# Performance work log

Measured on AMD Instinct MI355X. Metric: run time of the kernel, lower is better.

The kernel has to match this reference:

```python
import jax, jax.numpy as jnp
import numpy as np

B = 256      # batch size (molecules)
A = 64       # num_atoms per molecule
N = B * A    # total nodes = 16384
E = 262144   # num edges
H = 128      # hidden_dim
L = 4        # num_layers
LAT = 64     # latent_dim
AF = 16      # atom_feature_dim
LN_EPS = 1e-5


def setup_inputs() -> dict:
    key = jax.random.key(0)
    ks = jax.random.split(key, 26)
    w = lambda k, shape: (jax.random.normal(k, shape) * 0.05).astype(jnp.float32)
    inp = {}
    inp["z"] = jax.random.normal(ks[0], (B, LAT), jnp.float32)
    inp["atom_types"] = jax.nn.one_hot(
        jax.random.randint(ks[1], (N,), 0, AF), AF, dtype=jnp.float32)
    inp["pos0"] = jax.random.normal(ks[2], (N, 3), jnp.float32) * 0.1
    inp["edge_index"] = jax.random.randint(ks[3], (2, E), 0, N)
    # latent injector: Linear(LAT+AF, 2H) -> SiLU -> Linear(2H, H) -> SiLU -> Linear(H, H)
    inp["inj_W1"] = w(ks[4], (AF + LAT, 2 * H)); inp["inj_b1"] = jnp.zeros((2 * H,), jnp.float32)
    inp["inj_W2"] = w(ks[5], (2 * H, H));        inp["inj_b2"] = jnp.zeros((H,), jnp.float32)
    inp["inj_W3"] = w(ks[6], (H, H));            inp["inj_b3"] = jnp.zeros((H,), jnp.float32)
    # per-layer params, stacked over layer dim L
    inp["edge_W1"] = w(ks[7], (L, 2 * H + 1, H)); inp["edge_b1"] = jnp.zeros((L, H), jnp.float32)
    inp["edge_W2"] = w(ks[8], (L, H, H));         inp["edge_b2"] = jnp.zeros((L, H), jnp.float32)
    inp["coord_W1"] = w(ks[9], (L, H, H));        inp["coord_b1"] = jnp.zeros((L, H), jnp.float32)
    inp["coord_W2"] = w(ks[10], (L, H, 1))  # no bias
    inp["node_W1"] = w(ks[11], (L, 2 * H, H));    inp["node_b1"] = jnp.zeros((L, H), jnp.float32)
    inp["node_W2"] = w(ks[12], (L, H, H));        inp["node_b2"] = jnp.zeros((L, H), jnp.float32)
    inp["ln_g"] = jnp.ones((L, H), jnp.float32)
    inp["ln_b"] = jnp.zeros((L, H), jnp.float32)
    return inp


def _layer_norm(x, g, b):
    mu = jnp.mean(x, axis=-1, keepdims=True)
    var = jnp.mean((x - mu) ** 2, axis=-1, keepdims=True)
    return (x - mu) * jax.lax.rsqrt(var + LN_EPS) * g + b


def _egnn_layer(h, pos, row, col, eW1, eb1, eW2, eb2, cW1, cb1, cW2, nW1, nb1, nW2, nb2, g, b):
    # --- message: gather endpoints, edge MLP ---
    rel = pos[row] - pos[col]                                   # [E, 3]
    dsq = jnp.clip(jnp.sum(rel * rel, axis=1, keepdims=True), 1e-6, 1e6)  # [E, 1]
    ef = jnp.concatenate([h[row], h[col], dsq], axis=1)         # [E, 2H+1]
    m = jax.nn.silu(ef @ eW1 + eb1)
    m = jax.nn.silu(m @ eW2 + eb2)
    m = jnp.clip(m, -10.0, 10.0)                                # [E, H]
    # --- coordinate update: coord MLP -> weighted rel_pos -> scatter_add, mean-normalized ---
    cw = jax.nn.silu(m @ cW1 + cb1) @ cW2                       # [E, 1]
    coord_update = jax.ops.segment_sum(cw * rel, row, num_segments=N)   # [N, 3]
    num_neighbors = jax.ops.segment_sum(jnp.ones((row.shape[0],), m.dtype), row, num_segments=N)[:, None]
    pos_new = pos + coord_update / (num_neighbors + 1e-6)
    # --- node update: scatter_add messages, node MLP, residual + LayerNorm ---
    agg = jax.ops.segment_sum(m, row, num_segments=N)           # [N, H]
    nu = jnp.concatenate([h, agg], axis=1)                      # [N, 2H]
    nu = jax.nn.silu(nu @ nW1 + nb1) @ nW2 + nb2
    h_new = _layer_norm(h + nu, g, b)
    return h_new, pos_new


def reference(z, atom_types, pos0, edge_index,
              inj_W1, inj_b1, inj_W2, inj_b2, inj_W3, inj_b3,
              edge_W1, edge_b1, edge_W2, edge_b2,
              coord_W1, coord_b1, coord_W2,
              node_W1, node_b1, node_W2, node_b2,
              ln_g, ln_b):
    # latent injection: h = MLP(cat[atom_types, repeat_interleave(z, num_atoms)])
    z_exp = jnp.repeat(z, A, axis=0)                            # [N, LAT]
    h = jnp.concatenate([atom_types, z_exp], axis=1)            # [N, AF+LAT]
    h = jax.nn.silu(h @ inj_W1 + inj_b1)
    h = jax.nn.silu(h @ inj_W2 + inj_b2)
    h = h @ inj_W3 + inj_b3                                     # [N, H]
    pos = pos0
    row, col = edge_index[0], edge_index[1]
    for l in range(L):
        h, pos = _egnn_layer(h, pos, row, col,
                             edge_W1[l], edge_b1[l], edge_W2[l], edge_b2[l],
                             coord_W1[l], coord_b1[l], coord_W2[l],
                             node_W1[l], node_b1[l], node_W2[l], node_b2[l],
                             ln_g[l], ln_b[l])
    return pos
```

## Files before the change

### kernel.cpp

```cpp
#include <hip/hip_runtime.h>
#include <cmath>

#define N_NODES 16384
#define E_EDGES 262144
#define HD 128
#define NLAYER 4

typedef __attribute__((ext_vector_type(8))) short bf16x8;
typedef __attribute__((ext_vector_type(4))) float f32x4;
#define MFMA16(a, b, c) __builtin_amdgcn_mfma_f32_16x16x32_bf16(a, b, c, 0, 0, 0)

__device__ __forceinline__ float silu_f(float x) {
  return __fdividef(x, 1.0f + __expf(-x));
}

__device__ __forceinline__ unsigned short bf16_rn(float f) {
  union { float f; unsigned u; } v; v.f = f;
  unsigned r = (v.u + 0x7FFFu + ((v.u >> 16) & 1u)) >> 16;
  return (unsigned short)r;
}
__device__ __forceinline__ float bf16_tof(unsigned short h) {
  union { unsigned u; float f; } v; v.u = ((unsigned)h) << 16; return v.f;
}

__global__ void k_prep_w(const float* __restrict__ eW1, const float* __restrict__ eW2,
                         const float* __restrict__ cW1,
                         unsigned short* __restrict__ e1f, unsigned short* __restrict__ e2f,
                         unsigned short* __restrict__ c1f) {
  int sid = blockIdx.x * 256 + threadIdx.x;
  int layer = sid >> 13;
  int r = sid & 8191;
  const float* src; unsigned short* base; int c, s, halfstride;
  if (r < 4096) {
    c = r >> 9; s = r & 511;
    src = eW1 + (size_t)layer * 257 * 128;
    base = e1f + (size_t)layer * 65536; halfstride = 32768;
  } else if (r < 6144) {
    int rr = r - 4096; c = rr >> 9; s = rr & 511;
    src = eW2 + (size_t)layer * 128 * 128;
    base = e2f + (size_t)layer * 32768; halfstride = 16384;
  } else {
    int rr = r - 6144; c = rr >> 9; s = rr & 511;
    src = cW1 + (size_t)layer * 128 * 128;
    base = c1f + (size_t)layer * 32768; halfstride = 16384;
  }
  int cf = s >> 6, lp = s & 63;
  int n = cf * 16 + (lp & 15);
  int k0 = c * 32 + (lp >> 4) * 8;
  bf16x8 hv, lv;
#pragma unroll
  for (int j = 0; j < 8; ++j) {
    float w = src[(size_t)(k0 + j) * 128 + n];
    unsigned short h = bf16_rn(w);
    hv[j] = (short)h;
    lv[j] = (short)bf16_rn(w - bf16_tof(h));
  }
  size_t off = ((size_t)c * 512 + s) * 8;
  *(bf16x8*)(base + off) = hv;
  *(bf16x8*)(base + halfstride + off) = lv;
}

__global__ void k_h2bf(const float* __restrict__ h, unsigned short* __restrict__ hhi,
                       unsigned short* __restrict__ hlo) {
  int i = (blockIdx.x * 256 + threadIdx.x) * 8;
  float4 a = *(const float4*)(h + i), b = *(const float4*)(h + i + 4);
  float v[8] = {a.x, a.y, a.z, a.w, b.x, b.y, b.z, b.w};
  bf16x8 hv, lv;
#pragma unroll
  for (int j = 0; j < 8; ++j) {
    unsigned u = __float_as_uint(v[j]);
    hv[j] = (short)(u >> 16);
    float hi_f = __uint_as_float(u & 0xFFFF0000u);
    lv[j] = (short)bf16_rn(v[j] - hi_f);
  }
  *(bf16x8*)(hhi + i) = hv;
  *(bf16x8*)(hlo + i) = lv;
}

__global__ __launch_bounds__(256, 4) void k_edge_mfma(
    const unsigned short* __restrict__ hhi, const unsigned short* __restrict__ hlo,
    const float* __restrict__ pos,
    const int* __restrict__ rows, const int* __restrict__ cols, const int* __restrict__ perm,
    const unsigned short* __restrict__ e1f, const float* __restrict__ eW1,
    const float* __restrict__ eb1,
    const unsigned short* __restrict__ e2f, const float* __restrict__ eb2,
    const unsigned short* __restrict__ c1f, const float* __restrict__ cb1,
    const float* __restrict__ cW2,
    float* __restrict__ agg, float* __restrict__ coordacc) {
  __shared__ __align__(16) float T[64][132];
  __shared__ int srow[64], scol[64];
  __shared__ float sdsq[64];
  __shared__ float srel[64][4];

  const int tid = threadIdx.x;
  const int lane = tid & 63;
  const int w = tid >> 6;
  const int l15 = lane & 15, l4 = lane >> 4;
  const int j0 = blockIdx.x * 64;
  const f32x4 zero4 = {0.f, 0.f, 0.f, 0.f};

  if (tid < 64) {
    int e = perm[j0 + tid];
    int r = rows[e], c = cols[e];
    srow[tid] = r; scol[tid] = c;
    float rx = pos[r * 3 + 0] - pos[c * 3 + 0];
    float ry = pos[r * 3 + 1] - pos[c * 3 + 1];
    float rz = pos[r * 3 + 2] - pos[c * 3 + 2];
    srel[tid][0] = rx; srel[tid][1] = ry; srel[tid][2] = rz;
    float d = rx * rx + ry * ry + rz * rz;
    sdsq[tid] = fminf(fmaxf(d, 1e-6f), 1e6f);
  }
  __syncthreads();

  f32x4 acc[8];

#pragma unroll
  for (int i = 0; i < 8; ++i) acc[i] = zero4;
  for (int c = 0; c < 8; ++c) {
    int node = (c < 4 ? srow : scol)[16 * w + l15];
    int koff = (c & 3) * 32 + l4 * 8;
    bf16x8 ah = *(const bf16x8*)(hhi + (size_t)node * 128 + koff);
    bf16x8 al = *(const bf16x8*)(hlo + (size_t)node * 128 + koff);
    const unsigned short* b0 = e1f + (size_t)c * 4096 + (size_t)lane * 8;
#pragma unroll
    for (int cf = 0; cf < 8; ++cf) {
      bf16x8 bh = *(const bf16x8*)(b0 + cf * 512);
      bf16x8 bl = *(const bf16x8*)(b0 + 32768 + cf * 512);
      acc[cf] = MFMA16(ah, bh, acc[cf]);
      acc[cf] = MFMA16(al, bh, acc[cf]);
      acc[cf] = MFMA16(ah, bl, acc[cf]);
    }
  }
#pragma unroll
  for (int cf = 0; cf < 8; ++cf) {
    int col = cf * 16 + l15;
    float wl = eW1[256 * 128 + col];
    float bb = eb1[col];
#pragma unroll
    for (int r = 0; r < 4; ++r) {
      int trow = 16 * w + l4 * 4 + r;
      T[trow][col] = silu_f(acc[cf][r] + sdsq[trow] * wl + bb);
    }
  }

#pragma unroll
  for (int i = 0; i < 8; ++i) acc[i] = zero4;
  for (int c = 0; c < 4; ++c) {
    int trow = 16 * w + l15;
    int k0 = c * 32 + l4 * 8;
    float tv[8];
    *(float4*)(tv) = *(const float4*)(&T[trow][k0]);
    *(float4*)(tv + 4) = *(const float4*)(&T[trow][k0 + 4]);
    bf16x8 ah, al;
#pragma unroll
    for (int j = 0; j < 8; ++j) {
      unsigned u = __float_as_uint(tv[j]);
      ah[j] = (short)(u >> 16);
      float hi_f = __uint_as_float(u & 0xFFFF0000u);
      al[j] = (short)bf16_rn(tv[j] - hi_f);
    }
    const unsigned short* b0 = e2f + (size_t)c * 4096 + (size_t)lane * 8;
#pragma unroll
    for (int cf = 0; cf < 8; ++cf) {
      bf16x8 bh = *(const bf16x8*)(b0 + cf * 512);
      bf16x8 bl = *(const bf16x8*)(b0 + 16384 + cf * 512);
      acc[cf] = MFMA16(ah, bh, acc[cf]);
      acc[cf] = MFMA16(al, bh, acc[cf]);
      acc[cf] = MFMA16(ah, bl, acc[cf]);
    }
  }
#pragma unroll
  for (int cf = 0; cf < 8; ++cf) {
    int col = cf * 16 + l15;
    float bb = eb2[col];
#pragma unroll
    for (int r = 0; r < 4; ++r) {
      int trow = 16 * w + l4 * 4 + r;
      float v = silu_f(acc[cf][r] + bb);
      v = fminf(fmaxf(v, -10.0f), 10.0f);
      acc[cf][r] = v;
      T[trow][col] = v;
    }
  }
  {
    int seg = 0;
    while (seg < 16) {
      int node = srow[16 * w + seg];
      int se = seg + 1;
      while (se < 16 && srow[16 * w + se] == node) ++se;
#pragma unroll
      for (int cf = 0; cf < 8; ++cf) {
        float s = 0.f;
#pragma unroll
        for (int r = 0; r < 4; ++r) {
          int row = l4 * 4 + r;
          s += (row >= seg && row < se) ? acc[cf][r] : 0.f;
        }
        s += __shfl_xor(s, 16);
        s += __shfl_xor(s, 32);
        if (l4 == 0) atomicAdd(&agg[(size_t)node * 128 + cf * 16 + l15], s);
      }
      seg = se;
    }
  }

#pragma unroll
  for (int i = 0; i < 8; ++i) acc[i] = zero4;
  for (int c = 0; c < 4; ++c) {
    int trow = 16 * w + l15;
    int k0 = c * 32 + l4 * 8;
    float tv[8];
    *(float4*)(tv) = *(const float4*)(&T[trow][k0]);
    *(float4*)(tv + 4) = *(const float4*)(&T[trow][k0 + 4]);
    bf16x8 ah, al;
#pragma unroll
    for (int j = 0; j < 8; ++j) {
      unsigned u = __float_as_uint(tv[j]);
      ah[j] = (short)(u >> 16);
      float hi_f = __uint_as_float(u & 0xFFFF0000u);
      al[j] = (short)bf16_rn(tv[j] - hi_f);
    }
    const unsigned short* b0 = c1f + (size_t)c * 4096 + (size_t)lane * 8;
#pragma unroll
    for (int cf = 0; cf < 8; ++cf) {
      bf16x8 bh = *(const bf16x8*)(b0 + cf * 512);
      bf16x8 bl = *(const bf16x8*)(b0 + 16384 + cf * 512);
      acc[cf] = MFMA16(ah, bh, acc[cf]);
      acc[cf] = MFMA16(al, bh, acc[cf]);
      acc[cf] = MFMA16(ah, bl, acc[cf]);
    }
  }
  {
    float p[4] = {0.f, 0.f, 0.f, 0.f};
#pragma unroll
    for (int cf = 0; cf < 8; ++cf) {
      int col = cf * 16 + l15;
      float bb = cb1[col];
      float w2 = cW2[col];
#pragma unroll
      for (int r = 0; r < 4; ++r) p[r] += silu_f(acc[cf][r] + bb) * w2;
    }
#pragma unroll
    for (int d = 1; d < 16; d <<= 1) {
#pragma unroll
      for (int r = 0; r < 4; ++r) p[r] += __shfl_xor(p[r], d);
    }
    int seg = 0;
    while (seg < 16) {
      int node = srow[16 * w + seg];
      int se = seg + 1;
      while (se < 16 && srow[16 * w + se] == node) ++se;
      float s = 0.f;
      if (l15 < 3) {
#pragma unroll
        for (int r = 0; r < 4; ++r) {
          int row = l4 * 4 + r;
          s += (row >= seg && row < se) ? p[r] * srel[16 * w + row][l15] : 0.f;
        }
      }
      s += __shfl_xor(s, 16);
      s += __shfl_xor(s, 32);
      if (l4 == 0 && l15 < 3) atomicAdd(&coordacc[(size_t)node * 4 + l15], s);
      seg = se;
    }
  }
}

__global__ void k_pos_fin(const float* __restrict__ coordacc, const int* __restrict__ offs,
                          float* __restrict__ pos) {
  int n = blockIdx.x * 256 + threadIdx.x;
  if (n < N_NODES) {
    float deg = (float)(offs[n + 1] - offs[n]);
    float inv = __fdividef(1.0f, deg + 1e-6f);
    pos[n * 3 + 0] += coordacc[n * 4 + 0] * inv;
    pos[n * 3 + 1] += coordacc[n * 4 + 1] * inv;
    pos[n * 3 + 2] += coordacc[n * 4 + 2] * inv;
  }
}

template <int ACT>
__global__ __launch_bounds__(256, 2) void k_gemm128(const float* Ag, const float* __restrict__ W,
                                                    const float* __restrict__ bias, float* C, int K) {
  __shared__ float As[64][33];
  __shared__ float Ws[32][128];
  const int tid = threadIdx.x;
  const int tc = tid & 15, tr = tid >> 4;
  const int tr4 = tr * 4, tc4 = tc * 4;
  const int m0 = blockIdx.x * 64;

  float acc[4][8];
#pragma unroll
  for (int i = 0; i < 4; ++i)
#pragma unroll
    for (int j = 0; j < 8; ++j) acc[i][j] = 0.0f;

  for (int kk = 0; kk < K; kk += 32) {
    int idx = tid;
#pragma unroll
    for (int it = 0; it < 2; ++it, idx += 256) {
      int r = idx >> 3, c4 = (idx & 7) << 2;
      float4 v = *(const float4*)(Ag + (size_t)(m0 + r) * K + kk + c4);
      As[r][c4] = v.x; As[r][c4 + 1] = v.y; As[r][c4 + 2] = v.z; As[r][c4 + 3] = v.w;
    }
    idx = tid;
#pragma unroll
    for (int it = 0; it < 4; ++it, idx += 256) {
      int r = idx >> 5, c4 = (idx & 31) << 2;
      *(float4*)(&Ws[r][c4]) = *(const float4*)(W + (size_t)(kk + r) * 128 + c4);
    }
    __syncthreads();
#pragma unroll
    for (int k = 0; k < 32; ++k) {
      float av[4];
#pragma unroll
      for (int i = 0; i < 4; ++i) av[i] = As[tr4 + i][k];
      float4 b0 = *(const float4*)(&Ws[k][tc4]);
      float4 b1 = *(const float4*)(&Ws[k][64 + tc4]);
      float bv[8] = {b0.x, b0.y, b0.z, b0.w, b1.x, b1.y, b1.z, b1.w};
#pragma unroll
      for (int i = 0; i < 4; ++i)
#pragma unroll
        for (int j = 0; j < 8; ++j) acc[i][j] = fmaf(av[i], bv[j], acc[i][j]);
    }
    __syncthreads();
  }

  float bv0[8];
#pragma unroll
  for (int j = 0; j < 4; ++j) { bv0[j] = bias[tc4 + j]; bv0[4 + j] = bias[64 + tc4 + j]; }
#pragma unroll
  for (int i = 0; i < 4; ++i) {
    size_t row = m0 + tr4 + i;
    float o[8];
#pragma unroll
    for (int j = 0; j < 8; ++j) {
      float v = acc[i][j] + bv0[j];
      if (ACT >= 1) v = silu_f(v);
      o[j] = v;
    }
    *(float4*)(C + row * 128 + tc4) = make_float4(o[0], o[1], o[2], o[3]);
    *(float4*)(C + row * 128 + 64 + tc4) = make_float4(o[4], o[5], o[6], o[7]);
  }
}

__global__ void k_count(const int* __restrict__ rows, int* __restrict__ cnt) {
  int e = blockIdx.x * 256 + threadIdx.x;
  if (e < E_EDGES) atomicAdd(&cnt[rows[e]], 1);
}

__global__ void k_scan(const int* __restrict__ cnt, int* __restrict__ offs) {
  __shared__ int part[256];
  const int tid = threadIdx.x;
  const int base = tid * 64;
  int s = 0;
  for (int i = 0; i < 64; ++i) s += cnt[base + i];
  part[tid] = s;
  __syncthreads();
  for (int d = 1; d < 256; d <<= 1) {
    int v = (tid >= d) ? part[tid - d] : 0;
    __syncthreads();
    part[tid] += v;
    __syncthreads();
  }
  int run = part[tid] - s;
  for (int i = 0; i < 64; ++i) { offs[base + i] = run; run += cnt[base + i]; }
  if (tid == 255) offs[N_NODES] = run;
}

__global__ void k_fill(const int* __restrict__ rows, const int* __restrict__ offs,
                       int* __restrict__ fill, int* __restrict__ perm) {
  int e = blockIdx.x * 256 + threadIdx.x;
  if (e < E_EDGES) {
    int r = rows[e];
    int p = atomicAdd(&fill[r], 1);
    perm[offs[r] + p] = e;
  }
}

__global__ __launch_bounds__(256, 2) void k_node_mlp(float* __restrict__ h, const float* __restrict__ agg,
                                                     const float* __restrict__ W1, const float* __restrict__ b1,
                                                     const float* __restrict__ W2, const float* __restrict__ b2,
                                                     const float* __restrict__ lng, const float* __restrict__ lnb,
                                                     unsigned short* __restrict__ hhi,
                                                     unsigned short* __restrict__ hlo) {
  __shared__ float As[64][33];
  __shared__ float Ws[32][128];
  __shared__ float T[64][132];
  const int tid = threadIdx.x;
  const int tc = tid & 15, tr = tid >> 4;
  const int tr4 = tr * 4, tc4 = tc * 4;
  const int m0 = blockIdx.x * 64;

  float acc[4][8];
#pragma unroll
  for (int i = 0; i < 4; ++i)
#pragma unroll
    for (int j = 0; j < 8; ++j) acc[i][j] = 0.0f;

  for (int kk = 0; kk < 256; kk += 32) {
    const float* src = (kk < 128) ? h : agg;
    const int kb = kk & 127;
    int idx = tid;
#pragma unroll
    for (int it = 0; it < 2; ++it, idx += 256) {
      int r = idx >> 3, c4 = (idx & 7) << 2;
      float4 v = *(const float4*)(src + (size_t)(m0 + r) * 128 + kb + c4);
      As[r][c4] = v.x; As[r][c4 + 1] = v.y; As[r][c4 + 2] = v.z; As[r][c4 + 3] = v.w;
    }
    idx = tid;
#pragma unroll
    for (int it = 0; it < 4; ++it, idx += 256) {
      int r = idx >> 5, c4 = (idx & 31) << 2;
      *(float4*)(&Ws[r][c4]) = *(const float4*)(W1 + (size_t)(kk + r) * 128 + c4);
    }
    __syncthreads();
#pragma unroll
    for (int k = 0; k < 32; ++k) {
      float av[4];
#pragma unroll
      for (int i = 0; i < 4; ++i) av[i] = As[tr4 + i][k];
      float4 b0 = *(const float4*)(&Ws[k][tc4]);
      float4 b1v = *(const float4*)(&Ws[k][64 + tc4]);
      float bv[8] = {b0.x, b0.y, b0.z, b0.w, b1v.x, b1v.y, b1v.z, b1v.w};
#pragma unroll
      for (int i = 0; i < 4; ++i)
#pragma unroll
        for (int j = 0; j < 8; ++j) acc[i][j] = fmaf(av[i], bv[j], acc[i][j]);
    }
    __syncthreads();
  }
#pragma unroll
  for (int i = 0; i < 4; ++i) {
#pragma unroll
    for (int j = 0; j < 4; ++j) {
      T[tr4 + i][tc4 + j] = silu_f(acc[i][j] + b1[tc4 + j]);
      T[tr4 + i][64 + tc4 + j] = silu_f(acc[i][4 + j] + b1[64 + tc4 + j]);
    }
  }
  __syncthreads();

  float acc2[4][8];
#pragma unroll
  for (int i = 0; i < 4; ++i)
#pragma unroll
    for (int j = 0; j < 8; ++j) acc2[i][j] = 0.0f;
  for (int kk = 0; kk < 128; kk += 32) {
    int idx = tid;
#pragma unroll
    for (int it = 0; it < 4; ++it, idx += 256) {
      int r = idx >> 5, c4 = (idx & 31) << 2;
      *(float4*)(&Ws[r][c4]) = *(const float4*)(W2 + (size_t)(kk + r) * 128 + c4);
    }
    __syncthreads();
#pragma unroll
    for (int k = 0; k < 32; ++k) {
      float av[4];
#pragma unroll
      for (int i = 0; i < 4; ++i) av[i] = T[tr4 + i][kk + k];
      float4 b0 = *(const float4*)(&Ws[k][tc4]);
      float4 b1v = *(const float4*)(&Ws[k][64 + tc4]);
      float bv[8] = {b0.x, b0.y, b0.z, b0.w, b1v.x, b1v.y, b1v.z, b1v.w};
#pragma unroll
      for (int i = 0; i < 4; ++i)
#pragma unroll
        for (int j = 0; j < 8; ++j) acc2[i][j] = fmaf(av[i], bv[j], acc2[i][j]);
    }
    __syncthreads();
  }

  float x[4][8], s1[4], s2[4];
#pragma unroll
  for (int i = 0; i < 4; ++i) {
    size_t row = m0 + tr4 + i;
    float4 h0 = *(const float4*)(h + row * 128 + tc4);
    float4 h1 = *(const float4*)(h + row * 128 + 64 + tc4);
    float hv[8] = {h0.x, h0.y, h0.z, h0.w, h1.x, h1.y, h1.z, h1.w};
    s1[i] = 0.f; s2[i] = 0.f;
#pragma unroll
    for (int j = 0; j < 8; ++j) {
      int cidx = (j < 4) ? (tc4 + j) : (64 + tc4 + (j - 4));
      float v = hv[j] + acc2[i][j] + b2[cidx];
      x[i][j] = v;
      s1[i] += v;
      s2[i] += v * v;
    }
  }
#pragma unroll
  for (int d = 1; d < 16; d <<= 1) {
#pragma unroll
    for (int i = 0; i < 4; ++i) {
      s1[i] += __shfl_xor(s1[i], d);
      s2[i] += __shfl_xor(s2[i], d);
    }
  }
  float gv[8], bvv[8];
#pragma unroll
  for (int j = 0; j < 4; ++j) {
    gv[j] = lng[tc4 + j]; gv[4 + j] = lng[64 + tc4 + j];
    bvv[j] = lnb[tc4 + j]; bvv[4 + j] = lnb[64 + tc4 + j];
  }
#pragma unroll
  for (int i = 0; i < 4; ++i) {
    float mu = s1[i] * (1.0f / 128.0f);
    float var = s2[i] * (1.0f / 128.0f) - mu * mu;
    float rs = rsqrtf(var + 1e-5f);
    size_t row = m0 + tr4 + i;
    float o[8];
    unsigned hv16[8], lv16[8];
#pragma unroll
    for (int j = 0; j < 8; ++j) {
      o[j] = (x[i][j] - mu) * rs * gv[j] + bvv[j];
      unsigned u = __float_as_uint(o[j]);
      hv16[j] = u >> 16;
      lv16[j] = bf16_rn(o[j] - __uint_as_float(u & 0xFFFF0000u));
    }
    *(float4*)(h + row * 128 + tc4) = make_float4(o[0], o[1], o[2], o[3]);
    *(float4*)(h + row * 128 + 64 + tc4) = make_float4(o[4], o[5], o[6], o[7]);
    *(uint2*)(hhi + row * 128 + tc4) =
        make_uint2(hv16[0] | (hv16[1] << 16), hv16[2] | (hv16[3] << 16));
    *(uint2*)(hhi + row * 128 + 64 + tc4) =
        make_uint2(hv16[4] | (hv16[5] << 16), hv16[6] | (hv16[7] << 16));
    *(uint2*)(hlo + row * 128 + tc4) =
        make_uint2(lv16[0] | (lv16[1] << 16), lv16[2] | (lv16[3] << 16));
    *(uint2*)(hlo + row * 128 + 64 + tc4) =
        make_uint2(lv16[4] | (lv16[5] << 16), lv16[6] | (lv16[7] << 16));
  }
}

__global__ __launch_bounds__(256) void k_inj1(const float* __restrict__ at, const float* __restrict__ z,
                                              const float* __restrict__ W1, const float* __restrict__ b1,
                                              float* __restrict__ out) {
  __shared__ float As[64][84];
  __shared__ float Ws[80][128];
  const int tid = threadIdx.x;
  const int tc = tid & 15, tr = tid >> 4;
  const int tr4 = tr * 4, tc4 = tc * 4;
  const int m0 = blockIdx.y * 64;
  const int cb = blockIdx.x * 128;

  int idx = tid;
#pragma unroll
  for (int it = 0; it < 5; ++it, idx += 256) {
    int r = idx / 20, c4 = idx % 20;
    int n = m0 + r;
    float4 v;
    if (c4 < 4) v = *(const float4*)(at + (size_t)n * 16 + c4 * 4);
    else v = *(const float4*)(z + (size_t)(n >> 6) * 64 + (c4 - 4) * 4);
    *(float4*)(&As[r][c4 * 4]) = v;
  }
  idx = tid;
#pragma unroll
  for (int it = 0; it < 10; ++it, idx += 256) {
    int r = idx >> 5, c4 = (idx & 31) << 2;
    *(float4*)(&Ws[r][c4]) = *(const float4*)(W1 + (size_t)r * 256 + cb + c4);
  }
  __syncthreads();

  float acc[4][8];
#pragma unroll
  for (int i = 0; i < 4; ++i)
#pragma unroll
    for (int j = 0; j < 8; ++j) acc[i][j] = 0.0f;
#pragma unroll 4
  for (int k = 0; k < 80; ++k) {
    float av[4];
#pragma unroll
    for (int i = 0; i < 4; ++i) av[i] = As[tr4 + i][k];
    float4 b0 = *(const float4*)(&Ws[k][tc4]);
    float4 b1v = *(const float4*)(&Ws[k][64 + tc4]);
    float bv[8] = {b0.x, b0.y, b0.z, b0.w, b1v.x, b1v.y, b1v.z, b1v.w};
#pragma unroll
    for (int i = 0; i < 4; ++i)
#pragma unroll
      for (int j = 0; j < 8; ++j) acc[i][j] = fmaf(av[i], bv[j], acc[i][j]);
  }

  float bb[8];
#pragma unroll
  for (int j = 0; j < 4; ++j) { bb[j] = b1[cb + tc4 + j]; bb[4 + j] = b1[cb + 64 + tc4 + j]; }
#pragma unroll
  for (int i = 0; i < 4; ++i) {
    size_t row = m0 + tr4 + i;
    float o[8];
#pragma unroll
    for (int j = 0; j < 8; ++j) o[j] = silu_f(acc[i][j] + bb[j]);
    *(float4*)(out + row * 256 + cb + tc4) = make_float4(o[0], o[1], o[2], o[3]);
    *(float4*)(out + row * 256 + cb + 64 + tc4) = make_float4(o[4], o[5], o[6], o[7]);
  }
}

__global__ void k_copyf(const float* __restrict__ in, float* __restrict__ out, int n) {
  int i = blockIdx.x * 256 + threadIdx.x;
  if (i < n) out[i] = in[i];
}

extern "C" void kernel_launch(void* const* d_in, const int* in_sizes, int n_in,
                              void* d_out, int out_size, void* d_ws, size_t ws_size,
                              hipStream_t stream) {
  const float* z = (const float*)d_in[0];
  const float* at = (const float*)d_in[1];
  const float* pos0 = (const float*)d_in[2];
  const int* ei = (const int*)d_in[3];
  const float* injW1 = (const float*)d_in[4];
  const float* injb1 = (const float*)d_in[5];
  const float* injW2 = (const float*)d_in[6];
  const float* injb2 = (const float*)d_in[7];
  const float* injW3 = (const float*)d_in[8];
  const float* injb3 = (const float*)d_in[9];
  const float* eW1 = (const float*)d_in[10];
  const float* eb1 = (const float*)d_in[11];
  const float* eW2 = (const float*)d_in[12];
  const float* eb2 = (const float*)d_in[13];
  const float* cW1 = (const float*)d_in[14];
  const float* cb1 = (const float*)d_in[15];
  const float* cW2 = (const float*)d_in[16];
  const float* nW1 = (const float*)d_in[17];
  const float* nb1 = (const float*)d_in[18];
  const float* nW2 = (const float*)d_in[19];
  const float* nb2 = (const float*)d_in[20];
  const float* lng = (const float*)d_in[21];
  const float* lnb = (const float*)d_in[22];

  float* w = (float*)d_ws;
  float* h = w;        w += (size_t)N_NODES * HD;
  float* pos = w;      w += (size_t)N_NODES * 3;
  float* agg = w;      w += (size_t)N_NODES * HD;
  float* coordacc = w; w += (size_t)N_NODES * 4;
  float* t1 = w;       w += (size_t)N_NODES * 256;
  float* t2 = w;       w += (size_t)N_NODES * HD;
  unsigned short* hhi = (unsigned short*)w;
  unsigned short* hlo = hhi + (size_t)N_NODES * HD;
  unsigned short* e1f = hlo + (size_t)N_NODES * HD;
  unsigned short* e2f = e1f + (size_t)4 * 65536;
  unsigned short* c1f = e2f + (size_t)4 * 32768;
  int* ib = (int*)(c1f + (size_t)4 * 32768);
  int* cnt = ib;  ib += N_NODES;
  int* offs = ib; ib += N_NODES + 1;
  int* fill = ib; ib += N_NODES;
  int* perm = ib; ib += E_EDGES;

  const int* rowsp = ei;
  const int* colsp = ei + E_EDGES;

  hipMemsetAsync(cnt, 0, N_NODES * sizeof(int), stream);
  hipMemsetAsync(fill, 0, N_NODES * sizeof(int), stream);
  k_count<<<E_EDGES / 256, 256, 0, stream>>>(rowsp, cnt);
  k_scan<<<1, 256, 0, stream>>>(cnt, offs);
  k_fill<<<E_EDGES / 256, 256, 0, stream>>>(rowsp, offs, fill, perm);
  k_copyf<<<(N_NODES * 3 + 255) / 256, 256, 0, stream>>>(pos0, pos, N_NODES * 3);

  k_prep_w<<<128, 256, 0, stream>>>(eW1, eW2, cW1, e1f, e2f, c1f);

  k_inj1<<<dim3(2, N_NODES / 64), 256, 0, stream>>>(at, z, injW1, injb1, t1);
  k_gemm128<1><<<N_NODES / 64, 256, 0, stream>>>(t1, injW2, injb2, t2, 256);
  k_gemm128<0><<<N_NODES / 64, 256, 0, stream>>>(t2, injW3, injb3, h, 128);
  k_h2bf<<<(N_NODES * HD / 8) / 256, 256, 0, stream>>>(h, hhi, hlo);

  for (int l = 0; l < NLAYER; ++l) {
    hipMemsetAsync(agg, 0, (size_t)N_NODES * HD * sizeof(float), stream);
    hipMemsetAsync(coordacc, 0, (size_t)N_NODES * 4 * sizeof(float), stream);
    k_edge_mfma<<<E_EDGES / 64, 256, 0, stream>>>(
        hhi, hlo, pos, rowsp, colsp, perm,
        e1f + (size_t)l * 65536, eW1 + (size_t)l * 257 * HD, eb1 + l * HD,
        e2f + (size_t)l * 32768, eb2 + l * HD,
        c1f + (size_t)l * 32768, cb1 + l * HD,
        cW2 + (size_t)l * HD,
        agg, coordacc);
    k_pos_fin<<<N_NODES / 256, 256, 0, stream>>>(coordacc, offs, pos);
    k_node_mlp<<<N_NODES / 64, 256, 0, stream>>>(h, agg, nW1 + (size_t)l * 2 * HD * HD, nb1 + l * HD,
                                                 nW2 + (size_t)l * HD * HD, nb2 + l * HD,
                                                 lng + l * HD, lnb + l * HD, hhi, hlo);
  }
  k_copyf<<<(N_NODES * 3 + 255) / 256, 256, 0, stream>>>(pos, (float*)d_out, N_NODES * 3);
}
```

Before: 1.190 ms.

## Double-buffer edge MLP weight chunks into LDS via async global_load_lds

Stages each K-chunk of the bf16 hi/lo weight fragments for the three edge-kernel GEMMs into a double-buffered LDS array using global_load_lds, prefetching the next chunk while MFMAs consume the current one. Previously every wave fetched the weight fragments directly from global memory. The change adds 32KB of LDS per block, a __syncthreads per chunk, and lowers the occupancy hint from 4 to 2 blocks per CU. There is no explicit vmcnt wait before reading the staged data, so correctness depends on the barrier ordering the async loads.

New measurement: 1.262 ms. 6.0% more time.

```diff
diff --git a/kernel.cpp b/kernel.cpp
--- a/kernel.cpp
+++ b/kernel.cpp
@@ -9,6 +9,9 @@
 typedef __attribute__((ext_vector_type(8))) short bf16x8;
 typedef __attribute__((ext_vector_type(4))) float f32x4;
 #define MFMA16(a, b, c) __builtin_amdgcn_mfma_f32_16x16x32_bf16(a, b, c, 0, 0, 0)
+
+typedef __attribute__((address_space(1))) const void gconst_void;
+typedef __attribute__((address_space(3))) void lds_void;
 
 __device__ __forceinline__ float silu_f(float x) {
   return __fdividef(x, 1.0f + __expf(-x));
@@ -77,7 +80,7 @@
   *(bf16x8*)(hlo + i) = lv;
 }
 
-__global__ __launch_bounds__(256, 4) void k_edge_mfma(
+__global__ __launch_bounds__(256, 2) void k_edge_mfma(
     const unsigned short* __restrict__ hhi, const unsigned short* __restrict__ hlo,
     const float* __restrict__ pos,
     const int* __restrict__ rows, const int* __restrict__ cols, const int* __restrict__ perm,
@@ -88,6 +91,7 @@
     const float* __restrict__ cW2,
     float* __restrict__ agg, float* __restrict__ coordacc) {
   __shared__ __align__(16) float T[64][132];
+  __shared__ __align__(16) short Bl[2][2][4096];
   __shared__ int srow[64], scol[64];
   __shared__ float sdsq[64];
   __shared__ float srel[64][4];
@@ -98,6 +102,21 @@
   const int l15 = lane & 15, l4 = lane >> 4;
   const int j0 = blockIdx.x * 64;
   const f32x4 zero4 = {0.f, 0.f, 0.f, 0.f};
+
+  auto stage = [&](int d, const unsigned short* wsrc, int halfstride, int chunk) {
+#pragma unroll
+    for (int t = 0; t < 4; ++t) {
+      int idx0 = w * 64 + t * 256;
+      int half = idx0 >> 9;
+      int rem0 = idx0 & 511;
+      const unsigned short* g = wsrc + (size_t)half * halfstride +
+                                ((size_t)chunk * 512 + rem0 + lane) * 8;
+      short* l = &Bl[d][half][rem0 * 8];
+      __builtin_amdgcn_global_load_lds((gconst_void*)g, (lds_void*)l, 16, 0, 0);
+    }
+  };
+
+  stage(0, e1f, 32768, 0);
 
   if (tid < 64) {
     int e = perm[j0 + tid];
@@ -117,20 +136,24 @@
 #pragma unroll
   for (int i = 0; i < 8; ++i) acc[i] = zero4;
   for (int c = 0; c < 8; ++c) {
+    if (c < 7) stage((c + 1) & 1, e1f, 32768, c + 1);
+    const int cur = c & 1;
     int node = (c < 4 ? srow : scol)[16 * w + l15];
     int koff = (c & 3) * 32 + l4 * 8;
     bf16x8 ah = *(const bf16x8*)(hhi + (size_t)node * 128 + koff);
     bf16x8 al = *(const bf16x8*)(hlo + (size_t)node * 128 + koff);
-    const unsigned short* b0 = e1f + (size_t)c * 4096 + (size_t)lane * 8;
 #pragma unroll
     for (int cf = 0; cf < 8; ++cf) {
-      bf16x8 bh = *(const bf16x8*)(b0 + cf * 512);
-      bf16x8 bl = *(const bf16x8*)(b0 + 32768 + cf * 512);
+      bf16x8 bh = *(const bf16x8*)(&Bl[cur][0][cf * 512 + lane * 8]);
+      bf16x8 bl = *(const bf16x8*)(&Bl[cur][1][cf * 512 + lane * 8]);
       acc[cf] = MFMA16(ah, bh, acc[cf]);
       acc[cf] = MFMA16(al, bh, acc[cf]);
       acc[cf] = MFMA16(ah, bl, acc[cf]);
     }
-  }
+    __syncthreads();
+  }
+
+  stage(0, e2f, 16384, 0);
 #pragma unroll
   for (int cf = 0; cf < 8; ++cf) {
     int col = cf * 16 + l15;
@@ -142,10 +165,13 @@
       T[trow][col] = silu_f(acc[cf][r] + sdsq[trow] * wl + bb);
     }
   }
+  __syncthreads();
 
 #pragma unroll
   for (int i = 0; i < 8; ++i) acc[i] = zero4;
   for (int c = 0; c < 4; ++c) {
+    if (c < 3) stage((c + 1) & 1, e2f, 16384, c + 1);
+    const int cur = c & 1;
     int trow = 16 * w + l15;
     int k0 = c * 32 + l4 * 8;
     float tv[8];
@@ -159,16 +185,18 @@
       float hi_f = __uint_as_float(u & 0xFFFF0000u);
       al[j] = (short)bf16_rn(tv[j] - hi_f);
     }
-    const unsigned short* b0 = e2f + (size_t)c * 4096 + (size_t)lane * 8;
 #pragma unroll
     for (int cf = 0; cf < 8; ++cf) {
-      bf16x8 bh = *(const bf16x8*)(b0 + cf * 512);
-      bf16x8 bl = *(const bf16x8*)(b0 + 16384 + cf * 512);
+      bf16x8 bh = *(const bf16x8*)(&Bl[cur][0][cf * 512 + lane * 8]);
+      bf16x8 bl = *(const bf16x8*)(&Bl[cur][1][cf * 512 + lane * 8]);
       acc[cf] = MFMA16(ah, bh, acc[cf]);
       acc[cf] = MFMA16(al, bh, acc[cf]);
       acc[cf] = MFMA16(ah, bl, acc[cf]);
     }
-  }
+    __syncthreads();
+  }
+
+  stage(0, c1f, 16384, 0);
 #pragma unroll
   for (int cf = 0; cf < 8; ++cf) {
     int col = cf * 16 + l15;
@@ -203,10 +231,13 @@
       seg = se;
     }
   }
+  __syncthreads();
 
 #pragma unroll
   for (int i = 0; i < 8; ++i) acc[i] = zero4;
   for (int c = 0; c < 4; ++c) {
+    if (c < 3) stage((c + 1) & 1, c1f, 16384, c + 1);
+    const int cur = c & 1;
     int trow = 16 * w + l15;
     int k0 = c * 32 + l4 * 8;
     float tv[8];
@@ -220,15 +251,15 @@
       float hi_f = __uint_as_float(u & 0xFFFF0000u);
       al[j] = (short)bf16_rn(tv[j] - hi_f);
     }
-    const unsigned short* b0 = c1f + (size_t)c * 4096 + (size_t)lane * 8;
 #pragma unroll
     for (int cf = 0; cf < 8; ++cf) {
-      bf16x8 bh = *(const bf16x8*)(b0 + cf * 512);
-      bf16x8 bl = *(const bf16x8*)(b0 + 16384 + cf * 512);
+      bf16x8 bh = *(const bf16x8*)(&Bl[cur][0][cf * 512 + lane * 8]);
+      bf16x8 bl = *(const bf16x8*)(&Bl[cur][1][cf * 512 + lane * 8]);
       acc[cf] = MFMA16(ah, bh, acc[cf]);
       acc[cf] = MFMA16(al, bh, acc[cf]);
       acc[cf] = MFMA16(ah, bl, acc[cf]);
     }
+    __syncthreads();
   }
   {
     float p[4] = {0.f, 0.f, 0.f, 0.f};
```
